# Kernel tuning notes

Hardware: AMD Instinct MI355X
Metric: run time of the kernel (lower is better)

Reference implementation:

```python
import jax, jax.numpy as jnp
import numpy as np

NUM_NETS = 100_000
PINS_PER_NET = 5
NUM_PINS = NUM_NETS * PINS_PER_NET
XL, XH, YL, YH = 0.0, 1000.0, 0.0, 1000.0
NUM_BINS_X = 512
NUM_BINS_Y = 512
BIN_SIZE_X = (XH - XL) / NUM_BINS_X
BIN_SIZE_Y = (YH - YL) / NUM_BINS_Y
NUM_H_TRACKS = 100.0
NUM_V_TRACKS = 100.0
MAX_RATE = 2.0
MIN_RATE = 1.0 / MAX_RATE


def setup_inputs() -> dict:
    key = jax.random.key(0)
    k1, k2, k3 = jax.random.split(key, 3)
    px = jax.random.uniform(k1, (NUM_PINS,), jnp.float32, XL, XH)
    py = jax.random.uniform(k2, (NUM_PINS,), jnp.float32, YL, YH)
    pin_pos = jnp.concatenate([px, py])  # [2*num_pins]: x then y
    netpin_start = (jnp.arange(NUM_NETS + 1, dtype=jnp.int32) * PINS_PER_NET)
    flat_netpin = jax.random.permutation(k3, NUM_PINS).astype(jnp.int32)
    net_weights = jnp.ones((NUM_NETS,), jnp.float32)
    return {"pin_pos": pin_pos, "netpin_start": netpin_start,
            "flat_netpin": flat_netpin, "net_weights": net_weights}


def reference(pin_pos, netpin_start, flat_netpin, net_weights):
    num_pins = flat_netpin.shape[0]
    # segment id of each flat pin slot (which net it belongs to)
    seg = jnp.searchsorted(netpin_start, jnp.arange(num_pins, dtype=netpin_start.dtype), side="right") - 1
    x = pin_pos[flat_netpin]                     # [num_pins]
    y = pin_pos[num_pins + flat_netpin]          # [num_pins]
    # per-net bounding boxes
    x_min = jax.ops.segment_min(x, seg, num_segments=NUM_NETS)
    x_max = jax.ops.segment_max(x, seg, num_segments=NUM_NETS)
    y_min = jax.ops.segment_min(y, seg, num_segments=NUM_NETS)
    y_max = jax.ops.segment_max(y, seg, num_segments=NUM_NETS)
    # fractional overlap of each net bbox with each bin column/row
    ex = XL + BIN_SIZE_X * jnp.arange(NUM_BINS_X + 1, dtype=pin_pos.dtype)
    ey = YL + BIN_SIZE_Y * jnp.arange(NUM_BINS_Y + 1, dtype=pin_pos.dtype)
    ox = jnp.maximum(jnp.minimum(x_max[:, None], ex[None, 1:]) -
                     jnp.maximum(x_min[:, None], ex[None, :-1]), 0.0)  # [N, Bx]
    oy = jnp.maximum(jnp.minimum(y_max[:, None], ey[None, 1:]) -
                     jnp.maximum(y_min[:, None], ey[None, :-1]), 0.0)  # [N, By]
    # RUDY: horizontal density wt/(y_max-y_min), vertical density wt/(x_max-x_min)
    wh = net_weights / (y_max - y_min)
    wv = net_weights / (x_max - x_min)
    h_map = jnp.einsum("nx,ny->xy", ox * wh[:, None], oy)
    v_map = jnp.einsum("nx,ny->xy", ox * wv[:, None], oy)
    h_map = h_map * (1.0 / (BIN_SIZE_X * NUM_H_TRACKS))
    v_map = v_map * (1.0 / (BIN_SIZE_Y * NUM_V_TRACKS))
    route = jnp.maximum(jnp.abs(h_map), jnp.abs(v_map))
    return jnp.clip(route * route, MIN_RATE, MAX_RATE)
```

## Files before the change

kernel.cpp:

```cpp
#include <hip/hip_runtime.h>

#define NUM_NETS     100000
#define PINS_PER_NET 5
#define NUM_PINS     (NUM_NETS * PINS_PER_NET)
#define NB           512
#define BIN_H        1.953125f
#define INV_H        0.512f
#define OUT_SCALE    (1.0f / 195.3125f)

#define SW           8
#define NSTRIPES     (NB / SW)
#define CAP          24576

#define FXS          2097152.0f
#define INV_FXS      (1.0f / 2097152.0f)

__global__ void zero_kernel(int* __restrict__ gcur) {
    gcur[threadIdx.x] = 0;
}

__global__ __launch_bounds__(256) void bbox_emit_kernel(
        const float* __restrict__ pin_pos,
        const int*   __restrict__ flat_netpin,
        const float* __restrict__ net_weights,
        int* __restrict__ gcur,
        float4* __restrict__ bucket) {
    __shared__ int lcnt[NSTRIPES];
    __shared__ int lbase[NSTRIPES];
    int tid = threadIdx.x;
    if (tid < NSTRIPES) lcnt[tid] = 0;
    __syncthreads();

    int n = blockIdx.x * 256 + tid;
    bool valid = n < NUM_NETS;
    float xmn = 1e30f, xmx = -1e30f, ymn = 1e30f, ymx = -1e30f;
    float wh = 0.f, wv = 0.f;
    int kx1 = 0, kx2 = 0;
    if (valid) {
#pragma unroll
        for (int p = 0; p < PINS_PER_NET; ++p) {
            int pi  = flat_netpin[n * PINS_PER_NET + p];
            float x = pin_pos[pi];
            float y = pin_pos[NUM_PINS + pi];
            xmn = fminf(xmn, x); xmx = fmaxf(xmx, x);
            ymn = fminf(ymn, y); ymx = fmaxf(ymx, y);
        }
        float w = net_weights[n];
        wh = w / (ymx - ymn);
        wv = w / (xmx - xmn);
        kx1 = min(NB - 1, (int)(xmn * INV_H));
        kx2 = min(NB - 1, (int)(xmx * INV_H));
#pragma unroll
        for (int cx = 0; cx < 2; ++cx) {
            int kx = cx ? kx2 : kx1;
            int s0 = kx >> 3;
            atomicAdd(&lcnt[s0], 2);
            if (kx + 1 < NB && ((kx + 1) >> 3) != s0)
                atomicAdd(&lcnt[(kx + 1) >> 3], 2);
        }
    }
    __syncthreads();
    if (tid < NSTRIPES) {
        lbase[tid] = atomicAdd(&gcur[tid], lcnt[tid]);
        lcnt[tid] = 0;
    }
    __syncthreads();
    if (valid) {
#pragma unroll
        for (int cx = 0; cx < 2; ++cx) {
            int   kx = cx ? kx2 : kx1;
            float xc = cx ? xmx : xmn;
            int s0 = kx >> 3;
            int s1 = (kx + 1 < NB) ? ((kx + 1) >> 3) : s0;
#pragma unroll
            for (int cy = 0; cy < 2; ++cy) {
                float yc = cy ? ymx : ymn;
                float sg = ((cx ^ cy) ? -1.0f : 1.0f);
                float4 item = make_float4(xc, yc, sg * wh, sg * wv);
                {
                    int rank = atomicAdd(&lcnt[s0], 1);
                    int pos  = lbase[s0] + rank;
                    if (pos < CAP) bucket[(size_t)s0 * CAP + pos] = item;
                }
                if (s1 != s0) {
                    int rank = atomicAdd(&lcnt[s1], 1);
                    int pos  = lbase[s1] + rank;
                    if (pos < CAP) bucket[(size_t)s1 * CAP + pos] = item;
                }
            }
        }
    }
}

__global__ __launch_bounds__(1024) void stripe_kernel(
        const float4* __restrict__ bucket,
        const int* __restrict__ gcur,
        float* __restrict__ UpH, float* __restrict__ UpV,
        float* __restrict__ Th,  float* __restrict__ Tv) {
    __shared__ int   acc[2 * SW * NB];
    __shared__ float wsc[32];
    int st  = blockIdx.x;
    int tid = threadIdx.x;
    int x0  = st * SW;
    int* accH = acc;
    int* accV = acc + SW * NB;

    for (int k = tid; k < 2 * SW * NB; k += 1024) acc[k] = 0;
    __syncthreads();

    int cnt = min(gcur[st], CAP);
    const float4* bk = bucket + (size_t)st * CAP;
    for (int q = tid; q < cnt; q += 1024) {
        float4 it = bk[q];
        int kx = min(NB - 1, (int)(it.x * INV_H));
        int ky = min(NB - 1, (int)(it.y * INV_H));
        float dx0 = (kx + 1) * BIN_H - it.x;
        float dx1 = it.x - kx * BIN_H;
        float dy0 = (ky + 1) * BIN_H - it.y;
        float dy1 = it.y - ky * BIN_H;
        bool y1ok = (ky + 1) < NB;
        int c = kx - x0;
#pragma unroll
        for (int cc = 0; cc < 2; ++cc) {
            int col = c + cc;
            if ((unsigned)col < SW) {
                float dx = cc ? dx1 : dx0;
                int b = col * NB + ky;
                atomicAdd(&accH[b], __float2int_rn(it.z * dx * dy0 * FXS));
                atomicAdd(&accV[b], __float2int_rn(it.w * dx * dy0 * FXS));
                if (y1ok) {
                    atomicAdd(&accH[b + 1], __float2int_rn(it.z * dx * dy1 * FXS));
                    atomicAdd(&accV[b + 1], __float2int_rn(it.w * dx * dy1 * FXS));
                }
            }
        }
    }
    __syncthreads();

    float* fH = (float*)accH;
    float* fV = (float*)accV;
    for (int k = tid; k < 2 * SW * NB; k += 1024)
        ((float*)acc)[k] = (float)acc[k] * INV_FXS;
    __syncthreads();

    int half = tid >> 9;
    int y    = tid & 511;
    int lane = tid & 63;
    int wv16 = tid >> 6;
    int wrow0 = half * 8;
#pragma unroll
    for (int rp = 0; rp < 4; ++rp) {
        int row = rp * 2 + half;
        float vH = fH[row * NB + y];
        float vV = fV[row * NB + y];
#pragma unroll
        for (int o = 1; o < 64; o <<= 1) {
            float a = __shfl_up(vH, o);
            float b = __shfl_up(vV, o);
            if (lane >= o) { vH += a; vV += b; }
        }
        if (lane == 63) { wsc[wv16] = vH; wsc[16 + wv16] = vV; }
        __syncthreads();
        float oh = 0.f, ov = 0.f;
        for (int j = wrow0; j < wv16; ++j) { oh += wsc[j]; ov += wsc[16 + j]; }
        fH[row * NB + y] = vH + oh;
        fV[row * NB + y] = vV + ov;
        __syncthreads();
    }

    if (tid < NB) {
        float f = 0.f;
#pragma unroll
        for (int rr = 0; rr < SW; ++rr) {
            int i = rr * NB + tid;
            f += fH[i]; fH[i] = f;
        }
        Th[st * NB + tid] = f;
    } else {
        int yy = tid - NB;
        float f = 0.f;
#pragma unroll
        for (int rr = 0; rr < SW; ++rr) {
            int i = rr * NB + yy;
            f += fV[i]; fV[i] = f;
        }
        Tv[st * NB + yy] = f;
    }
    __syncthreads();

    for (int k = tid; k < SW * NB; k += 1024) {
        int rr = k >> 9, yy = k & (NB - 1);
        int gi = (x0 + rr) * NB + yy;
        UpH[gi] = fH[k];
        UpV[gi] = fV[k];
    }
}

__global__ __launch_bounds__(512) void finish_kernel(
        const float* __restrict__ UpH, const float* __restrict__ UpV,
        const float* __restrict__ Th,  const float* __restrict__ Tv,
        float* __restrict__ out) {
    int st = blockIdx.x;
    int y  = threadIdx.x;
    float offh = 0.f, offv = 0.f;
    for (int s2 = 0; s2 < st; ++s2) {
        offh += Th[s2 * NB + y];
        offv += Tv[s2 * NB + y];
    }
#pragma unroll
    for (int rr = 0; rr < SW; ++rr) {
        int i = (st * SW + rr) * NB + y;
        float h = fabsf(UpH[i] + offh) * OUT_SCALE;
        float v = fabsf(UpV[i] + offv) * OUT_SCALE;
        float m = fmaxf(h, v);
        out[i] = fminf(fmaxf(m * m, 0.5f), 2.0f);
    }
}

__global__ void scatter_kernel(const float* __restrict__ pin_pos,
                               const int*   __restrict__ flat_netpin,
                               const float* __restrict__ net_weights,
                               float* __restrict__ Uh,
                               float* __restrict__ Uv) {
    int n = blockIdx.x * blockDim.x + threadIdx.x;
    if (n >= NUM_NETS) return;
    float xmn = 1e30f, xmx = -1e30f, ymn = 1e30f, ymx = -1e30f;
#pragma unroll
    for (int p = 0; p < PINS_PER_NET; ++p) {
        int pi  = flat_netpin[n * PINS_PER_NET + p];
        float x = pin_pos[pi];
        float y = pin_pos[NUM_PINS + pi];
        xmn = fminf(xmn, x); xmx = fmaxf(xmx, x);
        ymn = fminf(ymn, y); ymx = fmaxf(ymx, y);
    }
    float w  = net_weights[n];
    float wh = w / (ymx - ymn), wv = w / (xmx - xmn);
    int kx1 = min(NB - 1, (int)(xmn * INV_H));
    int kx2 = min(NB - 1, (int)(xmx * INV_H));
    int ky1 = min(NB - 1, (int)(ymn * INV_H));
    int ky2 = min(NB - 1, (int)(ymx * INV_H));
    int   xi[4] = { kx1, kx1 + 1, kx2, kx2 + 1 };
    float xv[4] = { (kx1 + 1) * BIN_H - xmn,  xmn - kx1 * BIN_H,
                    xmx - (kx2 + 1) * BIN_H,  kx2 * BIN_H - xmx };
    int   yi[4] = { ky1, ky1 + 1, ky2, ky2 + 1 };
    float yv[4] = { (ky1 + 1) * BIN_H - ymn,  ymn - ky1 * BIN_H,
                    ymx - (ky2 + 1) * BIN_H,  ky2 * BIN_H - ymx };
#pragma unroll
    for (int a = 0; a < 4; ++a) {
        if (xi[a] >= NB) continue;
#pragma unroll
        for (int b2 = 0; b2 < 4; ++b2) {
            if (yi[b2] >= NB) continue;
            float prod = xv[a] * yv[b2];
            atomicAdd(&Uh[xi[a] * NB + yi[b2]], wh * prod);
            atomicAdd(&Uv[xi[a] * NB + yi[b2]], wv * prod);
        }
    }
}

__global__ void fb_rowscan_kernel(float* __restrict__ Uh, float* __restrict__ Uv) {
    __shared__ float sh[NB];
    __shared__ float sv[NB];
    int rr = blockIdx.x, t = threadIdx.x;
    sh[t] = Uh[rr * NB + t];
    sv[t] = Uv[rr * NB + t];
    __syncthreads();
#pragma unroll
    for (int off = 1; off < NB; off <<= 1) {
        float a = (t >= off) ? sh[t - off] : 0.0f;
        float b = (t >= off) ? sv[t - off] : 0.0f;
        __syncthreads();
        sh[t] += a; sv[t] += b;
        __syncthreads();
    }
    Uh[rr * NB + t] = sh[t];
    Uv[rr * NB + t] = sv[t];
}

__global__ void fb_colscan_kernel(const float* __restrict__ Uh,
                                  const float* __restrict__ Uv,
                                  float* __restrict__ out) {
    int t = blockIdx.x * blockDim.x + threadIdx.x;
    if (t >= NB) return;
    float sh = 0.f, sv = 0.f;
    for (int i = 0; i < NB; ++i) {
        sh += Uh[i * NB + t];
        sv += Uv[i * NB + t];
        float h = fabsf(sh) * OUT_SCALE;
        float v = fabsf(sv) * OUT_SCALE;
        float m = fmaxf(h, v);
        out[i * NB + t] = fminf(fmaxf(m * m, 0.5f), 2.0f);
    }
}

extern "C" void kernel_launch(void* const* d_in, const int* in_sizes, int n_in,
                              void* d_out, int out_size, void* d_ws, size_t ws_size,
                              hipStream_t stream) {
    const float* pin_pos     = (const float*)d_in[0];
    const int*   flat_netpin = (const int*)d_in[2];
    const float* net_weights = (const float*)d_in[3];
    float* out = (float*)d_out;
    float* ws  = (float*)d_ws;

    const size_t o_cur = 0;
    const size_t o_bkt = 64;
    const size_t o_Th  = o_bkt + (size_t)NSTRIPES * CAP * 4;
    const size_t o_Tv  = o_Th + (size_t)NSTRIPES * NB;
    const size_t o_UpH = o_Tv + (size_t)NSTRIPES * NB;
    const size_t o_UpV = o_UpH + (size_t)NB * NB;
    const size_t need  = o_UpV + (size_t)NB * NB;

    if (ws_size < need * sizeof(float)) {
        float* Uh = ws;
        float* Uv = ws + (size_t)NB * NB;
        hipMemsetAsync(ws, 0, 2 * (size_t)NB * NB * sizeof(float), stream);
        scatter_kernel<<<(NUM_NETS + 255) / 256, 256, 0, stream>>>(
            pin_pos, flat_netpin, net_weights, Uh, Uv);
        fb_rowscan_kernel<<<NB, NB, 0, stream>>>(Uh, Uv);
        fb_colscan_kernel<<<2, 256, 0, stream>>>(Uh, Uv, out);
        return;
    }

    int*    gcur   = (int*)(ws + o_cur);
    float4* bucket = (float4*)(ws + o_bkt);
    float*  Th     = ws + o_Th;
    float*  Tv     = ws + o_Tv;
    float*  UpH    = ws + o_UpH;
    float*  UpV    = ws + o_UpV;

    zero_kernel<<<1, NSTRIPES, 0, stream>>>(gcur);

    bbox_emit_kernel<<<(NUM_NETS + 255) / 256, 256, 0, stream>>>(
        pin_pos, flat_netpin, net_weights, gcur, bucket);

    stripe_kernel<<<NSTRIPES, 1024, 0, stream>>>(bucket, gcur, UpH, UpV, Th, Tv);

    finish_kernel<<<NSTRIPES, 512, 0, stream>>>(UpH, UpV, Th, Tv, out);
}
```

Before: 57.38 us.

## Split each stripe into four y-slices to raise block count in accumulation

The stripe accumulation kernel is split so that each of the 64 x-stripes is processed by four blocks, each owning a 128-row y-slice. This gives 256 blocks instead of 64 and a smaller shared accumulator per block. Every slice block still reads the whole stripe bucket and drops items outside its slice, so bucket reads grow fourfold. The 2D prefix sum now needs per-slice row and column totals, which the finish kernel combines with an extra warp scan and a loop over earlier slices.

```diff
diff --git a/kernel.cpp b/kernel.cpp
--- a/kernel.cpp
+++ b/kernel.cpp
@@ -11,6 +11,8 @@
 #define SW           8
 #define NSTRIPES     (NB / SW)
 #define CAP          24576
+#define NSL          4
+#define SLH2         128
 
 #define FXS          2097152.0f
 #define INV_FXS      (1.0f / 2097152.0f)
@@ -92,20 +94,26 @@
     }
 }
 
-__global__ __launch_bounds__(1024) void stripe_kernel(
+__global__ __launch_bounds__(1024) void slice_kernel(
         const float4* __restrict__ bucket,
         const int* __restrict__ gcur,
         float* __restrict__ UpH, float* __restrict__ UpV,
-        float* __restrict__ Th,  float* __restrict__ Tv) {
-    __shared__ int   acc[2 * SW * NB];
-    __shared__ float wsc[32];
-    int st  = blockIdx.x;
+        float* __restrict__ ctH, float* __restrict__ ctV,
+        float* __restrict__ rH,  float* __restrict__ rV) {
+    __shared__ int   acc[2 * SW * SLH2];
+    __shared__ float rtmp[16];
+    __shared__ float rsH[8], rsV[8];
+    __shared__ float wscH[8], wscV[8];
+    int bid = blockIdx.x;
+    int st  = bid >> 2;
+    int h   = bid & 3;
     int tid = threadIdx.x;
     int x0  = st * SW;
+    int y0  = h * SLH2;
     int* accH = acc;
-    int* accV = acc + SW * NB;
-
-    for (int k = tid; k < 2 * SW * NB; k += 1024) acc[k] = 0;
+    int* accV = acc + SW * SLH2;
+
+    for (int k = tid; k < 2 * SW * SLH2; k += 1024) acc[k] = 0;
     __syncthreads();
 
     int cnt = min(gcur[st], CAP);
@@ -114,23 +122,29 @@
         float4 it = bk[q];
         int kx = min(NB - 1, (int)(it.x * INV_H));
         int ky = min(NB - 1, (int)(it.y * INV_H));
+        int gy = ky - y0;
+        if ((unsigned)(gy + 1) > (unsigned)SLH2) continue;
         float dx0 = (kx + 1) * BIN_H - it.x;
         float dx1 = it.x - kx * BIN_H;
         float dy0 = (ky + 1) * BIN_H - it.y;
         float dy1 = it.y - ky * BIN_H;
-        bool y1ok = (ky + 1) < NB;
+        bool ok0 = (unsigned)gy < (unsigned)SLH2;
+        bool ok1 = (ky + 1 < NB) && ((unsigned)(gy + 1) < (unsigned)SLH2);
         int c = kx - x0;
 #pragma unroll
         for (int cc = 0; cc < 2; ++cc) {
             int col = c + cc;
             if ((unsigned)col < SW) {
                 float dx = cc ? dx1 : dx0;
-                int b = col * NB + ky;
-                atomicAdd(&accH[b], __float2int_rn(it.z * dx * dy0 * FXS));
-                atomicAdd(&accV[b], __float2int_rn(it.w * dx * dy0 * FXS));
-                if (y1ok) {
-                    atomicAdd(&accH[b + 1], __float2int_rn(it.z * dx * dy1 * FXS));
-                    atomicAdd(&accV[b + 1], __float2int_rn(it.w * dx * dy1 * FXS));
+                if (ok0) {
+                    int b = col * SLH2 + gy;
+                    atomicAdd(&accH[b], __float2int_rn(it.z * dx * dy0 * FXS));
+                    atomicAdd(&accV[b], __float2int_rn(it.w * dx * dy0 * FXS));
+                }
+                if (ok1) {
+                    int b = col * SLH2 + gy + 1;
+                    atomicAdd(&accH[b], __float2int_rn(it.z * dx * dy1 * FXS));
+                    atomicAdd(&accV[b], __float2int_rn(it.w * dx * dy1 * FXS));
                 }
             }
         }
@@ -139,80 +153,147 @@
 
     float* fH = (float*)accH;
     float* fV = (float*)accV;
-    for (int k = tid; k < 2 * SW * NB; k += 1024)
+    for (int k = tid; k < 2 * SW * SLH2; k += 1024)
         ((float*)acc)[k] = (float)acc[k] * INV_FXS;
     __syncthreads();
 
-    int half = tid >> 9;
-    int y    = tid & 511;
+    int row  = tid >> 7;
+    int ly   = tid & 127;
     int lane = tid & 63;
-    int wv16 = tid >> 6;
-    int wrow0 = half * 8;
-#pragma unroll
-    for (int rp = 0; rp < 4; ++rp) {
-        int row = rp * 2 + half;
-        float vH = fH[row * NB + y];
-        float vV = fV[row * NB + y];
+    int wh2  = (tid >> 6) & 1;
+
+    {
+        float v = fH[tid];
+#pragma unroll
+        for (int o = 1; o < 64; o <<= 1) v += __shfl_xor(v, o);
+        if (lane == 0) rtmp[tid >> 6] = v;
+        __syncthreads();
+        if (tid < 8) rsH[tid] = rtmp[2 * tid] + rtmp[2 * tid + 1];
+        __syncthreads();
+        v = fV[tid];
+#pragma unroll
+        for (int o = 1; o < 64; o <<= 1) v += __shfl_xor(v, o);
+        if (lane == 0) rtmp[tid >> 6] = v;
+        __syncthreads();
+        if (tid < 8) rsV[tid] = rtmp[2 * tid] + rtmp[2 * tid + 1];
+        __syncthreads();
+        if (tid == 0) {
+            float f = 0.f;
+#pragma unroll
+            for (int x = 0; x < SW; ++x) { f += rsH[x]; rH[(st * NSL + h) * SW + x] = f; }
+            f = 0.f;
+#pragma unroll
+            for (int x = 0; x < SW; ++x) { f += rsV[x]; rV[(st * NSL + h) * SW + x] = f; }
+        }
+    }
+
+    if (tid < SLH2) {
+        float s = 0.f;
+#pragma unroll
+        for (int x = 0; x < SW; ++x) s += fH[x * SLH2 + tid];
+        ctH[st * NB + y0 + tid] = s;
+    } else if (tid < 2 * SLH2) {
+        int yy = tid - SLH2;
+        float s = 0.f;
+#pragma unroll
+        for (int x = 0; x < SW; ++x) s += fV[x * SLH2 + yy];
+        ctV[st * NB + y0 + yy] = s;
+    }
+    __syncthreads();
+
+    {
+        float v = fH[tid];
 #pragma unroll
         for (int o = 1; o < 64; o <<= 1) {
-            float a = __shfl_up(vH, o);
-            float b = __shfl_up(vV, o);
-            if (lane >= o) { vH += a; vV += b; }
-        }
-        if (lane == 63) { wsc[wv16] = vH; wsc[16 + wv16] = vV; }
-        __syncthreads();
-        float oh = 0.f, ov = 0.f;
-        for (int j = wrow0; j < wv16; ++j) { oh += wsc[j]; ov += wsc[16 + j]; }
-        fH[row * NB + y] = vH + oh;
-        fV[row * NB + y] = vV + ov;
-        __syncthreads();
-    }
-
-    if (tid < NB) {
+            float a = __shfl_up(v, o);
+            if (lane >= o) v += a;
+        }
+        if (lane == 63 && wh2 == 0) wscH[row] = v;
+        float u = fV[tid];
+#pragma unroll
+        for (int o = 1; o < 64; o <<= 1) {
+            float a = __shfl_up(u, o);
+            if (lane >= o) u += a;
+        }
+        if (lane == 63 && wh2 == 0) wscV[row] = u;
+        __syncthreads();
+        if (wh2 == 1) { v += wscH[row]; u += wscV[row]; }
+        fH[tid] = v;
+        fV[tid] = u;
+        __syncthreads();
+    }
+
+    if (tid < SLH2) {
         float f = 0.f;
 #pragma unroll
-        for (int rr = 0; rr < SW; ++rr) {
-            int i = rr * NB + tid;
+        for (int x = 0; x < SW; ++x) {
+            int i = x * SLH2 + tid;
             f += fH[i]; fH[i] = f;
         }
-        Th[st * NB + tid] = f;
-    } else {
-        int yy = tid - NB;
+    } else if (tid < 2 * SLH2) {
+        int yy = tid - SLH2;
         float f = 0.f;
 #pragma unroll
-        for (int rr = 0; rr < SW; ++rr) {
-            int i = rr * NB + yy;
+        for (int x = 0; x < SW; ++x) {
+            int i = x * SLH2 + yy;
             f += fV[i]; fV[i] = f;
         }
-        Tv[st * NB + yy] = f;
-    }
-    __syncthreads();
-
-    for (int k = tid; k < SW * NB; k += 1024) {
-        int rr = k >> 9, yy = k & (NB - 1);
-        int gi = (x0 + rr) * NB + yy;
-        UpH[gi] = fH[k];
-        UpV[gi] = fV[k];
+    }
+    __syncthreads();
+
+    {
+        int gi = (x0 + row) * NB + y0 + ly;
+        UpH[gi] = fH[tid];
+        UpV[gi] = fV[tid];
     }
 }
 
 __global__ __launch_bounds__(512) void finish_kernel(
         const float* __restrict__ UpH, const float* __restrict__ UpV,
-        const float* __restrict__ Th,  const float* __restrict__ Tv,
+        const float* __restrict__ ctH, const float* __restrict__ ctV,
+        const float* __restrict__ rH,  const float* __restrict__ rV,
         float* __restrict__ out) {
+    __shared__ float wsc[16];
     int st = blockIdx.x;
     int y  = threadIdx.x;
-    float offh = 0.f, offv = 0.f;
+    int lane = y & 63, wid = y >> 6;
+
+    float colH = 0.f, colV = 0.f;
     for (int s2 = 0; s2 < st; ++s2) {
-        offh += Th[s2 * NB + y];
-        offv += Tv[s2 * NB + y];
-    }
-#pragma unroll
-    for (int rr = 0; rr < SW; ++rr) {
-        int i = (st * SW + rr) * NB + y;
-        float h = fabsf(UpH[i] + offh) * OUT_SCALE;
-        float v = fabsf(UpV[i] + offv) * OUT_SCALE;
-        float m = fmaxf(h, v);
+        colH += ctH[s2 * NB + y];
+        colV += ctV[s2 * NB + y];
+    }
+#pragma unroll
+    for (int o = 1; o < 64; o <<= 1) {
+        float a = __shfl_up(colH, o);
+        float b = __shfl_up(colV, o);
+        if (lane >= o) { colH += a; colV += b; }
+    }
+    if (lane == 63) { wsc[wid] = colH; wsc[8 + wid] = colV; }
+    __syncthreads();
+    float oh = 0.f, ov = 0.f;
+    for (int j = 0; j < wid; ++j) { oh += wsc[j]; ov += wsc[8 + j]; }
+    float AH = colH + oh;
+    float AV = colV + ov;
+
+    int h = y >> 7;
+    float rpH[SW], rpV[SW];
+#pragma unroll
+    for (int x = 0; x < SW; ++x) { rpH[x] = 0.f; rpV[x] = 0.f; }
+    for (int h2 = 0; h2 < h; ++h2) {
+#pragma unroll
+        for (int x = 0; x < SW; ++x) {
+            rpH[x] += rH[(st * NSL + h2) * SW + x];
+            rpV[x] += rV[(st * NSL + h2) * SW + x];
+        }
+    }
+
+#pragma unroll
+    for (int x = 0; x < SW; ++x) {
+        int i = (st * SW + x) * NB + y;
+        float hv = fabsf(UpH[i] + rpH[x] + AH) * OUT_SCALE;
+        float vv = fabsf(UpV[i] + rpV[x] + AV) * OUT_SCALE;
+        float m = fmaxf(hv, vv);
         out[i] = fminf(fmaxf(m * m, 0.5f), 2.0f);
     }
 }
@@ -304,9 +385,11 @@
 
     const size_t o_cur = 0;
     const size_t o_bkt = 64;
-    const size_t o_Th  = o_bkt + (size_t)NSTRIPES * CAP * 4;
-    const size_t o_Tv  = o_Th + (size_t)NSTRIPES * NB;
-    const size_t o_UpH = o_Tv + (size_t)NSTRIPES * NB;
+    const size_t o_ctH = o_bkt + (size_t)NSTRIPES * CAP * 4;
+    const size_t o_ctV = o_ctH + (size_t)NSTRIPES * NB;
+    const size_t o_rH  = o_ctV + (size_t)NSTRIPES * NB;
+    const size_t o_rV  = o_rH + (size_t)NSTRIPES * NSL * SW;
+    const size_t o_UpH = o_rV + (size_t)NSTRIPES * NSL * SW;
     const size_t o_UpV = o_UpH + (size_t)NB * NB;
     const size_t need  = o_UpV + (size_t)NB * NB;
 
@@ -323,8 +406,10 @@
 
     int*    gcur   = (int*)(ws + o_cur);
     float4* bucket = (float4*)(ws + o_bkt);
-    float*  Th     = ws + o_Th;
-    float*  Tv     = ws + o_Tv;
+    float*  ctH    = ws + o_ctH;
+    float*  ctV    = ws + o_ctV;
+    float*  rH     = ws + o_rH;
+    float*  rV     = ws + o_rV;
     float*  UpH    = ws + o_UpH;
     float*  UpV    = ws + o_UpV;
 
@@ -333,7 +418,8 @@
     bbox_emit_kernel<<<(NUM_NETS + 255) / 256, 256, 0, stream>>>(
         pin_pos, flat_netpin, net_weights, gcur, bucket);
 
-    stripe_kernel<<<NSTRIPES, 1024, 0, stream>>>(bucket, gcur, UpH, UpV, Th, Tv);
-
-    finish_kernel<<<NSTRIPES, 512, 0, stream>>>(UpH, UpV, Th, Tv, out);
-}
+    slice_kernel<<<NSTRIPES * NSL, 1024, 0, stream>>>(
+        bucket, gcur, UpH, UpV, ctH, ctV, rH, rV);
+
+    finish_kernel<<<NSTRIPES, 512, 0, stream>>>(UpH, UpV, ctH, ctV, rH, rV, out);
+}
```

Result: slower. 59.59 us (+3.9%).

## Fuse stripe and finish kernels using cross-block flag synchronization

Applied to the files above, without the earlier changes.

Merges the stripe prefix-sum kernel and the finish kernel into one launch. Each stripe block publishes its column totals and raises a flag, then spin-waits on the flags of earlier stripes and adds their totals in shared memory before writing the final output directly. This removes one kernel launch and the global round trip through the UpH/UpV intermediate maps, and folds the int-to-float conversion into the scan load. It relies on all 64 blocks being co-resident to avoid deadlock, and the zero kernel is widened so it also clears the flags.

```diff
diff --git a/kernel.cpp b/kernel.cpp
--- a/kernel.cpp
+++ b/kernel.cpp
@@ -92,18 +92,23 @@
     }
 }
 
-__global__ __launch_bounds__(1024) void stripe_kernel(
+__global__ __launch_bounds__(1024) void stripe_finish_kernel(
         const float4* __restrict__ bucket,
         const int* __restrict__ gcur,
-        float* __restrict__ UpH, float* __restrict__ UpV,
-        float* __restrict__ Th,  float* __restrict__ Tv) {
+        float* __restrict__ Th,  float* __restrict__ Tv,
+        int* __restrict__ flag,
+        float* __restrict__ out) {
     __shared__ int   acc[2 * SW * NB];
     __shared__ float wsc[32];
+    __shared__ float offHs[2][NB];
+    __shared__ float offVs[2][NB];
     int st  = blockIdx.x;
     int tid = threadIdx.x;
     int x0  = st * SW;
     int* accH = acc;
     int* accV = acc + SW * NB;
+    float* fH = (float*)accH;
+    float* fV = (float*)accV;
 
     for (int k = tid; k < 2 * SW * NB; k += 1024) acc[k] = 0;
     __syncthreads();
@@ -137,12 +142,6 @@
     }
     __syncthreads();
 
-    float* fH = (float*)accH;
-    float* fV = (float*)accV;
-    for (int k = tid; k < 2 * SW * NB; k += 1024)
-        ((float*)acc)[k] = (float)acc[k] * INV_FXS;
-    __syncthreads();
-
     int half = tid >> 9;
     int y    = tid & 511;
     int lane = tid & 63;
@@ -151,8 +150,8 @@
 #pragma unroll
     for (int rp = 0; rp < 4; ++rp) {
         int row = rp * 2 + half;
-        float vH = fH[row * NB + y];
-        float vV = fV[row * NB + y];
+        float vH = (float)accH[row * NB + y] * INV_FXS;
+        float vV = (float)accV[row * NB + y] * INV_FXS;
 #pragma unroll
         for (int o = 1; o < 64; o <<= 1) {
             float a = __shfl_up(vH, o);
@@ -175,7 +174,8 @@
             int i = rr * NB + tid;
             f += fH[i]; fH[i] = f;
         }
-        Th[st * NB + tid] = f;
+        __hip_atomic_store(&Th[st * NB + tid], f, __ATOMIC_RELAXED,
+                           __HIP_MEMORY_SCOPE_AGENT);
     } else {
         int yy = tid - NB;
         float f = 0.f;
@@ -184,36 +184,45 @@
             int i = rr * NB + yy;
             f += fV[i]; fV[i] = f;
         }
-        Tv[st * NB + yy] = f;
-    }
-    __syncthreads();
-
-    for (int k = tid; k < SW * NB; k += 1024) {
-        int rr = k >> 9, yy = k & (NB - 1);
-        int gi = (x0 + rr) * NB + yy;
-        UpH[gi] = fH[k];
-        UpV[gi] = fV[k];
-    }
-}
-
-__global__ __launch_bounds__(512) void finish_kernel(
-        const float* __restrict__ UpH, const float* __restrict__ UpV,
-        const float* __restrict__ Th,  const float* __restrict__ Tv,
-        float* __restrict__ out) {
-    int st = blockIdx.x;
-    int y  = threadIdx.x;
-    float offh = 0.f, offv = 0.f;
-    for (int s2 = 0; s2 < st; ++s2) {
-        offh += Th[s2 * NB + y];
-        offv += Tv[s2 * NB + y];
-    }
-#pragma unroll
-    for (int rr = 0; rr < SW; ++rr) {
-        int i = (st * SW + rr) * NB + y;
-        float h = fabsf(UpH[i] + offh) * OUT_SCALE;
-        float v = fabsf(UpV[i] + offv) * OUT_SCALE;
-        float m = fmaxf(h, v);
-        out[i] = fminf(fmaxf(m * m, 0.5f), 2.0f);
+        __hip_atomic_store(&Tv[st * NB + yy], f, __ATOMIC_RELAXED,
+                           __HIP_MEMORY_SCOPE_AGENT);
+    }
+    __syncthreads();
+    if (tid == 0) {
+        __threadfence();
+        __hip_atomic_store(&flag[st], 1, __ATOMIC_RELEASE,
+                           __HIP_MEMORY_SCOPE_AGENT);
+    }
+
+    if (tid < st) {
+        while (__hip_atomic_load(&flag[tid], __ATOMIC_ACQUIRE,
+                                 __HIP_MEMORY_SCOPE_AGENT) == 0) { }
+    }
+    __syncthreads();
+    {
+        float sh = 0.f, sv = 0.f;
+        for (int s2 = half; s2 < st; s2 += 2) {
+            sh += __hip_atomic_load(&Th[s2 * NB + y], __ATOMIC_RELAXED,
+                                    __HIP_MEMORY_SCOPE_AGENT);
+            sv += __hip_atomic_load(&Tv[s2 * NB + y], __ATOMIC_RELAXED,
+                                    __HIP_MEMORY_SCOPE_AGENT);
+        }
+        offHs[half][y] = sh;
+        offVs[half][y] = sv;
+    }
+    __syncthreads();
+
+    {
+        float offh = offHs[0][y] + offHs[1][y];
+        float offv = offVs[0][y] + offVs[1][y];
+#pragma unroll
+        for (int r2 = 0; r2 < 4; ++r2) {
+            int rr = half * 4 + r2;
+            float h = fabsf(fH[rr * NB + y] + offh) * OUT_SCALE;
+            float v = fabsf(fV[rr * NB + y] + offv) * OUT_SCALE;
+            float m = fmaxf(h, v);
+            out[(x0 + rr) * NB + y] = fminf(fmaxf(m * m, 0.5f), 2.0f);
+        }
     }
 }
 
@@ -303,12 +312,11 @@
     float* ws  = (float*)d_ws;
 
     const size_t o_cur = 0;
-    const size_t o_bkt = 64;
+    const size_t o_flg = 64;
+    const size_t o_bkt = 128;
     const size_t o_Th  = o_bkt + (size_t)NSTRIPES * CAP * 4;
     const size_t o_Tv  = o_Th + (size_t)NSTRIPES * NB;
-    const size_t o_UpH = o_Tv + (size_t)NSTRIPES * NB;
-    const size_t o_UpV = o_UpH + (size_t)NB * NB;
-    const size_t need  = o_UpV + (size_t)NB * NB;
+    const size_t need  = o_Tv + (size_t)NSTRIPES * NB;
 
     if (ws_size < need * sizeof(float)) {
         float* Uh = ws;
@@ -322,18 +330,16 @@
     }
 
     int*    gcur   = (int*)(ws + o_cur);
+    int*    flg    = (int*)(ws + o_flg);
     float4* bucket = (float4*)(ws + o_bkt);
     float*  Th     = ws + o_Th;
     float*  Tv     = ws + o_Tv;
-    float*  UpH    = ws + o_UpH;
-    float*  UpV    = ws + o_UpV;
-
-    zero_kernel<<<1, NSTRIPES, 0, stream>>>(gcur);
+
+    zero_kernel<<<1, 128, 0, stream>>>(gcur);
 
     bbox_emit_kernel<<<(NUM_NETS + 255) / 256, 256, 0, stream>>>(
         pin_pos, flat_netpin, net_weights, gcur, bucket);
 
-    stripe_kernel<<<NSTRIPES, 1024, 0, stream>>>(bucket, gcur, UpH, UpV, Th, Tv);
-
-    finish_kernel<<<NSTRIPES, 512, 0, stream>>>(UpH, UpV, Th, Tv, out);
-}
+    stripe_finish_kernel<<<NSTRIPES, 1024, 0, stream>>>(
+        bucket, gcur, Th, Tv, flg, out);
+}
```

New measurement: 50.56 us. 1.13x faster.
